# Optimization experiments

Hardware: AMD Instinct MI355X
Metric: run time of the kernel (lower is better)

The kernel has to match this reference:

```python
import jax, jax.numpy as jnp
import numpy as np

B, N, D = 2, 2048, 1024
H = 16
HD = D // H
SCALE = HD ** -0.5


def setup_inputs() -> dict:
    key = jax.random.key(0)
    k1, k2, kw, kb = jax.random.split(key, 4)
    x1 = jax.random.normal(k1, (B, N, D), dtype=jnp.float32)
    x2 = jax.random.normal(k2, (B, N, D), dtype=jnp.float32)
    # fused qkv linear: torch nn.Linear(dim, 3*dim): W [3D, D], b [3D]
    bound = 1.0 / np.sqrt(D)
    qkv_w = jax.random.uniform(kw, (3 * D, D), minval=-bound, maxval=bound, dtype=jnp.float32)
    qkv_b = jax.random.uniform(kb, (3 * D,), minval=-bound, maxval=bound, dtype=jnp.float32)
    return {"x1": x1, "x2": x2, "qkv_w": qkv_w, "qkv_b": qkv_b}


def reference(x1, x2, qkv_w, qkv_b):
    # qkv projections (only q from x1 and k,v from x2 are used by the module)
    q1 = (jnp.einsum('bnd,ed->bne', x1, qkv_w[:D]) + qkv_b[:D])
    k2 = (jnp.einsum('bnd,ed->bne', x2, qkv_w[D:2 * D]) + qkv_b[D:2 * D])
    v2 = (jnp.einsum('bnd,ed->bne', x2, qkv_w[2 * D:]) + qkv_b[2 * D:])
    # [B, H, N, HD]
    q1 = q1.reshape(B, N, H, HD).transpose(0, 2, 1, 3)
    k2 = k2.reshape(B, N, H, HD).transpose(0, 2, 1, 3)
    v2 = v2.reshape(B, N, H, HD).transpose(0, 2, 1, 3)
    # explicit QK^T -> softmax -> AV (materializes [B,H,N,N] like the original)
    scores = jnp.einsum('bhqd,bhkd->bhqk', q1, k2) * SCALE
    attn = jax.nn.softmax(scores, axis=-1)
    out = jnp.einsum('bhqk,bhkd->bhqd', attn, v2)
    # [B, N, D]; note original module skips out_proj (never applied in forward)
    return out.transpose(0, 2, 1, 3).reshape(B, N, D)
```

## Files before the change

### kernel.cpp

```cpp
#include <hip/hip_runtime.h>
#include <cstdint>
#include <cstddef>

#define B_   2
#define N_   2048
#define D_   1024
#define H_   16
#define HD_  64
#define QSCALE_ 0.18033688011112042f

typedef unsigned short u16;
typedef unsigned int   u32;
typedef __attribute__((ext_vector_type(8))) short short8;
typedef __attribute__((ext_vector_type(4))) float f32x4;
typedef __attribute__((ext_vector_type(16))) float f32x16;
typedef __attribute__((ext_vector_type(4))) float fl4;
typedef __attribute__((ext_vector_type(4))) unsigned short us4;
typedef __attribute__((ext_vector_type(4))) unsigned int u32x4;

#if __has_builtin(__builtin_amdgcn_exp2f)
#define EXP2F(x) __builtin_amdgcn_exp2f(x)
#else
#define EXP2F(x) exp2f(x)
#endif

__device__ __forceinline__ u16 f2bf(float f) {
  u32 u = __builtin_bit_cast(u32, f);
  u += 0x7fffu + ((u >> 16) & 1u);
  return (u16)(u >> 16);
}

__device__ __forceinline__ u32 cvtpk(float lo, float hi) {
  u32 r;
  asm("v_cvt_pk_bf16_f32 %0, %1, %2" : "=v"(r) : "v"(lo), "v"(hi));
  return r;
}

__device__ __forceinline__ void plswap(u32& a, u32& b) {
  asm volatile("v_permlane32_swap_b32 %0, %1" : "+v"(a), "+v"(b));
}

__device__ __forceinline__ void gload16(const void* g, void* l) {
  typedef __attribute__((address_space(1))) unsigned int gu32;
  typedef __attribute__((address_space(3))) unsigned int lu32;
  __builtin_amdgcn_global_load_lds((gu32*)g, (lu32*)l, 16, 0, 0);
}

__global__ void convert_kernel(const fl4* __restrict__ x1, const fl4* __restrict__ x2,
                               const fl4* __restrict__ w,
                               us4* __restrict__ o1, us4* __restrict__ o2,
                               us4* __restrict__ ow) {
  const int NX = (B_ * N_ * D_) / 4;
  const int NW = (3 * D_ * D_) / 4;
  int stride = gridDim.x * blockDim.x;
  for (int i = blockIdx.x * blockDim.x + threadIdx.x; i < NX; i += stride) {
    fl4 a = x1[i];
    us4 r; r.x = f2bf(a.x); r.y = f2bf(a.y); r.z = f2bf(a.z); r.w = f2bf(a.w);
    o1[i] = r;
    fl4 b = x2[i];
    us4 s; s.x = f2bf(b.x); s.y = f2bf(b.y); s.z = f2bf(b.z); s.w = f2bf(b.w);
    o2[i] = s;
    if (i < NW) {
      fl4 c = w[i];
      us4 t; t.x = f2bf(c.x); t.y = f2bf(c.y); t.z = f2bf(c.z); t.w = f2bf(c.w);
      ow[i] = t;
    }
  }
}

__global__ __launch_bounds__(256) void qkv_gemm(
    const u16* __restrict__ x1b, const u16* __restrict__ x2b,
    const u16* __restrict__ wb, const float* __restrict__ bias,
    u16* __restrict__ Qb, u16* __restrict__ Kb, u16* __restrict__ Vtb) {
  const int z = blockIdx.z;
  const u16* X = (z == 0) ? x1b : x2b;
  const u16* W = wb + (size_t)z * D_ * D_;
  const float* bz = bias + z * D_;
  const int m0 = blockIdx.y * 128;
  const int e0 = blockIdx.x * 128;
  const int tid = threadIdx.x;
  const int lane = tid & 63;
  const int w = tid >> 6;
  const int wr = w >> 1, wc = w & 1;
  const int col = lane & 15, quad = lane >> 4;

  __shared__ __align__(16) u16 As[128 * 64];
  __shared__ __align__(16) u16 Bs[128 * 64];

  f32x4 acc[4][4] = {};

  const int cg = (lane & 7) ^ (lane >> 3);
  const u16* sA = X + (size_t)(m0 + w * 8 + (lane >> 3)) * D_ + cg * 8;
  const u16* sB = W + (size_t)(e0 + w * 8 + (lane >> 3)) * D_ + cg * 8;
  u16* dA = &As[w * 512];
  u16* dB = &Bs[w * 512];

  const int pg = (quad ^ (col & 7)) * 8;

  for (int k0 = 0; k0 < D_; k0 += 64) {
    __syncthreads();
#pragma unroll
    for (int rr = 0; rr < 4; ++rr) {
      gload16(sA + (size_t)rr * 32 * D_ + k0, dA + rr * 2048);
      gload16(sB + (size_t)rr * 32 * D_ + k0, dB + rr * 2048);
    }
    __syncthreads();

    short8 a[4][2], b[4][2];
#pragma unroll
    for (int i = 0; i < 4; ++i) {
      const int rb = (wr * 64 + i * 16 + col) * 64;
      a[i][0] = *(const short8*)&As[rb + pg];
      a[i][1] = *(const short8*)&As[rb + (pg ^ 32)];
    }
#pragma unroll
    for (int j = 0; j < 4; ++j) {
      const int rb = (wc * 64 + j * 16 + col) * 64;
      b[j][0] = *(const short8*)&Bs[rb + pg];
      b[j][1] = *(const short8*)&Bs[rb + (pg ^ 32)];
    }
    __builtin_amdgcn_s_setprio(1);
#pragma unroll
    for (int i = 0; i < 4; ++i)
#pragma unroll
      for (int j = 0; j < 4; ++j) {
        acc[i][j] = __builtin_amdgcn_mfma_f32_16x16x32_bf16(a[i][0], b[j][0], acc[i][j], 0, 0, 0);
        acc[i][j] = __builtin_amdgcn_mfma_f32_16x16x32_bf16(a[i][1], b[j][1], acc[i][j], 0, 0, 0);
      }
    __builtin_amdgcn_s_setprio(0);
  }

#pragma unroll
  for (int j = 0; j < 4; ++j) {
    int eg = e0 + wc * 64 + j * 16 + col;
    float bj = bz[eg];
    int h = eg >> 6, d = eg & 63;
#pragma unroll
    for (int i = 0; i < 4; ++i) {
#pragma unroll
      for (int r = 0; r < 4; ++r) {
        int m = m0 + wr * 64 + i * 16 + quad * 4 + r;
        int bb = m >> 11, n = m & (N_ - 1);
        float v = acc[i][j][r] + bj;
        if (z == 0) v *= QSCALE_;
        u16 o = f2bf(v);
        if (z == 0)      Qb [(((size_t)bb * H_ + h) * N_ + n) * HD_ + d] = o;
        else if (z == 1) Kb [(((size_t)bb * H_ + h) * N_ + n) * HD_ + d] = o;
        else             Vtb[(((size_t)bb * H_ + h) * HD_ + d) * N_ + n] = o;
      }
    }
  }
}

__global__ __launch_bounds__(256, 2) void attn_kernel(
    const u16* __restrict__ Qb, const u16* __restrict__ Kb,
    const u16* __restrict__ Vtb, float* __restrict__ out) {
  const int bh = blockIdx.y;
  const int bb = bh >> 4, h = bh & 15;
  const int q0 = blockIdx.x * 128;
  const int tid = threadIdx.x;
  const int lane = tid & 63;
  const int w = tid >> 6;
  const int l31 = lane & 31, hf = lane >> 5, r7 = lane & 7;

  const u16* __restrict__ Q  = Qb  + ((size_t)bh << 17);
  const u16* __restrict__ K  = Kb  + ((size_t)bh << 17);
  const u16* __restrict__ Vt = Vtb + ((size_t)bh << 17);

  __shared__ __align__(16) u16 Ks[2][64 * 64];
  __shared__ __align__(16) u16 Vs[2][64 * 64];
  __shared__ float Ls[4][32];

  const u16* Qr = Q + (size_t)(q0 + w * 32 + l31) * HD_;
  short8 qf[4];
#pragma unroll
  for (int c = 0; c < 4; ++c)
    qf[c] = *(const short8*)&Qr[c * 16 + hf * 8];

  const int srow = tid >> 3;
  const int sg   = tid & 7;
  const int lw0 = srow * 64 + ((sg ^ (srow & 7)) * 8);
  const int lw1 = lw0 + 2048;
  const u16* gK = K + tid * 8;
  const u16* gV = Vt + srow * N_ + sg * 8;

  f32x16 accO[2] = {};
  float lsum = 0.f;

  short8 kA = *(const short8*)(gK);
  short8 kB = *(const short8*)(gK + 2048);
  short8 vA = *(const short8*)(gV);
  short8 vB = *(const short8*)(gV + 32 * N_);
  *(short8*)&Ks[0][lw0] = kA;
  *(short8*)&Ks[0][lw1] = kB;
  *(short8*)&Vs[0][lw0] = vA;
  *(short8*)&Vs[0][lw1] = vB;

  for (int t = 0; t < N_ / 64; ++t) {
    __syncthreads();
    const int cur = t & 1;
    if (t < N_ / 64 - 1) {
      const int k0n = (t + 1) * 64;
      kA = *(const short8*)(gK + k0n * 64);
      kB = *(const short8*)(gK + k0n * 64 + 2048);
      vA = *(const short8*)(gV + k0n);
      vB = *(const short8*)(gV + k0n + 32 * N_);
    }
    const u16* Kc = Ks[cur];
    const u16* Vc = Vs[cur];

    f32x16 sT[2] = {};
    __builtin_amdgcn_s_setprio(1);
#pragma unroll
    for (int kb = 0; kb < 2; ++kb) {
      const int rb = (kb * 32 + l31) * 64;
#pragma unroll
      for (int c = 0; c < 4; ++c) {
        short8 kf = *(const short8*)&Kc[rb + (((c * 2 + hf) ^ r7) * 8)];
        sT[kb] = __builtin_amdgcn_mfma_f32_32x32x16_bf16(kf, qf[c], sT[kb], 0, 0, 0);
      }
    }
    __builtin_amdgcn_s_setprio(0);

#pragma unroll
    for (int kb = 0; kb < 2; ++kb)
#pragma unroll
      for (int i = 0; i < 16; ++i) {
        float e = EXP2F(sT[kb][i]);
        lsum += e;
        sT[kb][i] = e;
      }

    short8 pf[4];
#pragma unroll
    for (int kc = 0; kc < 4; ++kc) {
      const int kb = kc >> 1, o = (kc & 1) * 8;
      u32 X = cvtpk(sT[kb][o + 0], sT[kb][o + 1]);
      u32 Y = cvtpk(sT[kb][o + 4], sT[kb][o + 5]);
      plswap(X, Y);
      u32 Z = cvtpk(sT[kb][o + 2], sT[kb][o + 3]);
      u32 W = cvtpk(sT[kb][o + 6], sT[kb][o + 7]);
      plswap(Z, W);
      u32x4 pw = {X, Z, Y, W};
      pf[kc] = __builtin_bit_cast(short8, pw);
    }

    __builtin_amdgcn_s_setprio(1);
#pragma unroll
    for (int db = 0; db < 2; ++db) {
      const int rb = (db * 32 + l31) * 64;
#pragma unroll
      for (int kc = 0; kc < 4; ++kc) {
        short8 vf = *(const short8*)&Vc[rb + (((kc * 2 + hf) ^ r7) * 8)];
        accO[db] = __builtin_amdgcn_mfma_f32_32x32x16_bf16(pf[kc], vf, accO[db], 0, 0, 0);
      }
    }
    __builtin_amdgcn_s_setprio(0);

    if (t < N_ / 64 - 1) {
      u16* Kn = (u16*)Ks[cur ^ 1];
      u16* Vn = (u16*)Vs[cur ^ 1];
      *(short8*)&Kn[lw0] = kA;
      *(short8*)&Kn[lw1] = kB;
      *(short8*)&Vn[lw0] = vA;
      *(short8*)&Vn[lw1] = vB;
    }
  }

  lsum += __shfl_xor(lsum, 32);
  if (hf == 0) Ls[w][l31] = 1.0f / lsum;
  __syncthreads();

  float rinv[16];
#pragma unroll
  for (int r = 0; r < 16; ++r)
    rinv[r] = Ls[w][(r & 3) + 8 * (r >> 2) + 4 * hf];

#pragma unroll
  for (int db = 0; db < 2; ++db)
#pragma unroll
    for (int r = 0; r < 16; ++r) {
      int n = q0 + w * 32 + (r & 3) + 8 * (r >> 2) + 4 * hf;
      int e = h * HD_ + db * 32 + l31;
      out[((size_t)bb * N_ + n) * D_ + e] = accO[db][r] * rinv[r];
    }
}

extern "C" void kernel_launch(void* const* d_in, const int* in_sizes, int n_in,
                              void* d_out, int out_size, void* d_ws, size_t ws_size,
                              hipStream_t stream) {
  const float* x1 = (const float*)d_in[0];
  const float* x2 = (const float*)d_in[1];
  const float* qw = (const float*)d_in[2];
  const float* qb = (const float*)d_in[3];
  float* out = (float*)d_out;

  u16* ws   = (u16*)d_ws;
  u16* x1b  = ws;
  u16* x2b  = ws + 4194304;
  u16* wb   = ws + 8388608;
  u16* Qbf  = ws + 11534336;
  u16* Kbf  = ws + 15728640;
  u16* Vtb  = ws + 19922944;
  if (ws_size < (size_t)24117248 * 2) return;

  convert_kernel<<<dim3(1024), dim3(256), 0, stream>>>(
      (const fl4*)x1, (const fl4*)x2, (const fl4*)qw,
      (us4*)x1b, (us4*)x2b, (us4*)wb);

  qkv_gemm<<<dim3(8, 32, 3), dim3(256), 0, stream>>>(
      x1b, x2b, wb, qb, Qbf, Kbf, Vtb);

  attn_kernel<<<dim3(16, 32), dim3(256), 0, stream>>>(Qbf, Kbf, Vtb, out);
}
```

Measured before the change: 170.7 us.

## Enlarge QKV GEMM tiles to 256x256 and double-buffer LDS with interleaved prefetch

```diff
diff --git a/kernel.cpp b/kernel.cpp
--- a/kernel.cpp
+++ b/kernel.cpp
@@ -68,78 +68,109 @@
   }
 }
 
-__global__ __launch_bounds__(256) void qkv_gemm(
+__global__ __launch_bounds__(512, 2) void qkv_gemm(
     const u16* __restrict__ x1b, const u16* __restrict__ x2b,
     const u16* __restrict__ wb, const float* __restrict__ bias,
     u16* __restrict__ Qb, u16* __restrict__ Kb, u16* __restrict__ Vtb) {
-  const int z = blockIdx.z;
+  const int bx = blockIdx.x;
+  const int z   = bx >> 6;
+  const int rem = bx & 63;
+  const int m0  = (rem >> 2) * 256;
+  const int e0  = (rem & 3) * 256;
+
   const u16* X = (z == 0) ? x1b : x2b;
   const u16* W = wb + (size_t)z * D_ * D_;
   const float* bz = bias + z * D_;
-  const int m0 = blockIdx.y * 128;
-  const int e0 = blockIdx.x * 128;
   const int tid = threadIdx.x;
   const int lane = tid & 63;
   const int w = tid >> 6;
-  const int wr = w >> 1, wc = w & 1;
+  const int wm = w >> 2, wn = w & 3;
   const int col = lane & 15, quad = lane >> 4;
 
-  __shared__ __align__(16) u16 As[128 * 64];
-  __shared__ __align__(16) u16 Bs[128 * 64];
-
-  f32x4 acc[4][4] = {};
+  __shared__ __align__(16) u16 As[2][256 * 64];
+  __shared__ __align__(16) u16 Bs[2][256 * 64];
+
+  f32x4 acc[8][4] = {};
 
   const int cg = (lane & 7) ^ (lane >> 3);
   const u16* sA = X + (size_t)(m0 + w * 8 + (lane >> 3)) * D_ + cg * 8;
   const u16* sB = W + (size_t)(e0 + w * 8 + (lane >> 3)) * D_ + cg * 8;
-  u16* dA = &As[w * 512];
-  u16* dB = &Bs[w * 512];
+  const int dbase = w * 512;
 
   const int pg = (quad ^ (col & 7)) * 8;
 
-  for (int k0 = 0; k0 < D_; k0 += 64) {
+#define QSTAGE_A(nb, rr, kk) \
+  gload16(sA + (size_t)(rr) * 64 * D_ + (kk), &As[nb][(rr) * 4096 + dbase])
+#define QSTAGE_B(nb, rr, kk) \
+  gload16(sB + (size_t)(rr) * 64 * D_ + (kk), &Bs[nb][(rr) * 4096 + dbase])
+
+#define QPH(mlo)                                                              \
+  do {                                                                        \
+    short8 a0[2], a1[2];                                                      \
+    _Pragma("unroll")                                                         \
+    for (int mi = 0; mi < 2; ++mi) {                                          \
+      const int rb = (wm * 128 + ((mlo) + mi) * 16 + col) * 64;               \
+      a0[mi] = *(const short8*)&Ac[rb + pg];                                  \
+      a1[mi] = *(const short8*)&Ac[rb + (pg ^ 32)];                           \
+    }                                                                         \
+    __builtin_amdgcn_s_setprio(1);                                            \
+    _Pragma("unroll")                                                         \
+    for (int mi = 0; mi < 2; ++mi)                                            \
+      _Pragma("unroll")                                                       \
+      for (int j = 0; j < 4; ++j) {                                           \
+        acc[(mlo) + mi][j] = __builtin_amdgcn_mfma_f32_16x16x32_bf16(         \
+            a0[mi], bfr[j][0], acc[(mlo) + mi][j], 0, 0, 0);                  \
+        acc[(mlo) + mi][j] = __builtin_amdgcn_mfma_f32_16x16x32_bf16(         \
+            a1[mi], bfr[j][1], acc[(mlo) + mi][j], 0, 0, 0);                  \
+      }                                                                       \
+    __builtin_amdgcn_s_setprio(0);                                            \
+  } while (0)
+
+#pragma unroll
+  for (int rr = 0; rr < 4; ++rr) QSTAGE_A(0, rr, 0);
+#pragma unroll
+  for (int rr = 0; rr < 4; ++rr) QSTAGE_B(0, rr, 0);
+  __syncthreads();
+
+  for (int t = 0; t < D_ / 64; ++t) {
+    const int cb = t & 1, nb = cb ^ 1;
+    const int k0n = (t + 1) * 64;
+    const bool pf = (t < D_ / 64 - 1);
+    const u16* Ac = As[cb];
+    const u16* Bc = Bs[cb];
+
+    if (pf) { QSTAGE_A(nb, 0, k0n); QSTAGE_A(nb, 1, k0n); }
+    short8 bfr[4][2];
+#pragma unroll
+    for (int j = 0; j < 4; ++j) {
+      const int rb = (wn * 64 + j * 16 + col) * 64;
+      bfr[j][0] = *(const short8*)&Bc[rb + pg];
+      bfr[j][1] = *(const short8*)&Bc[rb + (pg ^ 32)];
+    }
+    QPH(0);
+    if (pf) { QSTAGE_A(nb, 2, k0n); QSTAGE_A(nb, 3, k0n); }
+    QPH(2);
+    if (pf) { QSTAGE_B(nb, 0, k0n); QSTAGE_B(nb, 1, k0n); }
+    QPH(4);
+    if (pf) { QSTAGE_B(nb, 2, k0n); QSTAGE_B(nb, 3, k0n); }
+    QPH(6);
+
     __syncthreads();
-#pragma unroll
-    for (int rr = 0; rr < 4; ++rr) {
-      gload16(sA + (size_t)rr * 32 * D_ + k0, dA + rr * 2048);
-      gload16(sB + (size_t)rr * 32 * D_ + k0, dB + rr * 2048);
-    }
-    __syncthreads();
-
-    short8 a[4][2], b[4][2];
-#pragma unroll
-    for (int i = 0; i < 4; ++i) {
-      const int rb = (wr * 64 + i * 16 + col) * 64;
-      a[i][0] = *(const short8*)&As[rb + pg];
-      a[i][1] = *(const short8*)&As[rb + (pg ^ 32)];
-    }
-#pragma unroll
-    for (int j = 0; j < 4; ++j) {
-      const int rb = (wc * 64 + j * 16 + col) * 64;
-      b[j][0] = *(const short8*)&Bs[rb + pg];
-      b[j][1] = *(const short8*)&Bs[rb + (pg ^ 32)];
-    }
-    __builtin_amdgcn_s_setprio(1);
-#pragma unroll
-    for (int i = 0; i < 4; ++i)
-#pragma unroll
-      for (int j = 0; j < 4; ++j) {
-        acc[i][j] = __builtin_amdgcn_mfma_f32_16x16x32_bf16(a[i][0], b[j][0], acc[i][j], 0, 0, 0);
-        acc[i][j] = __builtin_amdgcn_mfma_f32_16x16x32_bf16(a[i][1], b[j][1], acc[i][j], 0, 0, 0);
-      }
-    __builtin_amdgcn_s_setprio(0);
   }
+#undef QSTAGE_A
+#undef QSTAGE_B
+#undef QPH
 
 #pragma unroll
   for (int j = 0; j < 4; ++j) {
-    int eg = e0 + wc * 64 + j * 16 + col;
+    int eg = e0 + wn * 64 + j * 16 + col;
     float bj = bz[eg];
     int h = eg >> 6, d = eg & 63;
 #pragma unroll
-    for (int i = 0; i < 4; ++i) {
+    for (int i = 0; i < 8; ++i) {
 #pragma unroll
       for (int r = 0; r < 4; ++r) {
-        int m = m0 + wr * 64 + i * 16 + quad * 4 + r;
+        int m = m0 + wm * 128 + i * 16 + quad * 4 + r;
         int bb = m >> 11, n = m & (N_ - 1);
         float v = acc[i][j][r] + bj;
         if (z == 0) v *= QSCALE_;
@@ -308,7 +339,7 @@
       (const fl4*)x1, (const fl4*)x2, (const fl4*)qw,
       (us4*)x1b, (us4*)x2b, (us4*)wb);
 
-  qkv_gemm<<<dim3(8, 32, 3), dim3(256), 0, stream>>>(
+  qkv_gemm<<<dim3(192), dim3(512), 0, stream>>>(
       x1b, x2b, wb, qb, Qbf, Kbf, Vtb);
 
   attn_kernel<<<dim3(16, 32), dim3(256), 0, stream>>>(Qbf, Kbf, Vtb, out);
```

Result: slower. 194.3 us (+13.8%).
